# Optimization experiments

Hardware: AMD Instinct MI355X
Metric: run time of the kernel (lower is better)

## Reference

```python
import jax, jax.numpy as jnp
import numpy as np

H = 128   # hidden_size
E = 300   # embedding_dim
VOC = 32000
B, TP, TC = 8, 160, 160
D2 = 2 * H  # bidirectional feature dim


def gru_dir(x, Wih, Whh, bih, bhh, reverse):
    # x: [B,T,I] -> hidden states [B,T,Hs]; torch GRU gate order (r,z,n)
    Hs = Whh.shape[1]
    xg = jnp.einsum('bti,gi->btg', x, Wih) + bih  # [B,T,3Hs]
    if reverse:
        xg = xg[:, ::-1]
    def step(h, xt):
        gh = h @ Whh.T + bhh
        xr, xz, xn = jnp.split(xt, 3, axis=-1)
        hr, hz, hn = jnp.split(gh, 3, axis=-1)
        r = jax.nn.sigmoid(xr + hr)
        z = jax.nn.sigmoid(xz + hz)
        n = jnp.tanh(xn + r * hn)
        h = (1.0 - z) * n + z * h
        return h, h
    h0 = jnp.zeros((x.shape[0], Hs), x.dtype)
    _, hs = jax.lax.scan(step, h0, jnp.swapaxes(xg, 0, 1))
    hs = jnp.swapaxes(hs, 0, 1)
    if reverse:
        hs = hs[:, ::-1]
    return hs


def bigru(x, Wf, Uf, bif, bhf, Wb, Ub, bib, bhb):
    return jnp.concatenate([
        gru_dir(x, Wf, Uf, bif, bhf, False),
        gru_dir(x, Wb, Ub, bib, bhb, True)], axis=-1)


def setup_inputs() -> dict:
    key = jax.random.key(0)
    ks = iter(jax.random.split(key, 64))
    def rn(shape, s=0.05):
        return jax.random.normal(next(ks), shape, jnp.float32) * s
    inp = {}
    inp['text_a'] = jax.random.randint(next(ks), (B, TP), 0, VOC)
    inp['text_b'] = jax.random.randint(next(ks), (B, TC), 0, VOC)
    inp['emb'] = rn((VOC, E), 0.1)
    for pfx, ins in [('p', E), ('c', E), ('a', 6 * D2)]:
        for d in ('f', 'b'):
            inp[pfx + '_Wih_' + d] = rn((3 * H, ins))
            inp[pfx + '_Whh_' + d] = rn((3 * H, H))
            inp[pfx + '_bih_' + d] = jnp.zeros((3 * H,), jnp.float32)
            inp[pfx + '_bhh_' + d] = jnp.zeros((3 * H,), jnp.float32)
    inp['Wc1'] = rn((H, D2)); inp['Wc2'] = rn((H, D2)); inp['Vc'] = rn((H,))
    inp['Wb'] = rn((D2, D2))
    inp['Wd'] = rn((H, D2)); inp['Vd'] = rn((H,))
    inp['Wm'] = rn((H, D2)); inp['Vm'] = rn((H,))
    inp['Ws'] = rn((H, D2)); inp['Vs'] = rn((H,))
    inp['Wp'] = rn((H, D2)); inp['Vp'] = rn((H,))
    inp['W1'] = rn((H, D2)); inp['W2'] = rn((H, D2)); inp['Vv'] = rn((H,))
    inp['Wout'] = rn((2, D2)); inp['bout'] = jnp.zeros((2,), jnp.float32)
    return inp


def _forward(text_a, text_b, emb,
             p_Wih_f, p_Whh_f, p_bih_f, p_bhh_f, p_Wih_b, p_Whh_b, p_bih_b, p_bhh_b,
             c_Wih_f, c_Whh_f, c_bih_f, c_bhh_f, c_Wih_b, c_Whh_b, c_bih_b, c_bhh_b,
             a_Wih_f, a_Whh_f, a_bih_f, a_bhh_f, a_Wih_b, a_Whh_b, a_bih_b, a_bhh_b,
             Wc1, Wc2, Vc, Wb, Wd, Vd, Wm, Vm, Ws, Vs, Wp, Vp, W1, W2, Vv, Wout, bout):
    hp = bigru(emb[text_a], p_Wih_f, p_Whh_f, p_bih_f, p_bhh_f,
               p_Wih_b, p_Whh_b, p_bih_b, p_bhh_b)          # [B,Tp,2H]
    hc = bigru(emb[text_b], c_Wih_f, c_Whh_f, c_bih_f, c_bhh_f,
               c_Wih_b, c_Whh_b, c_bih_b, c_bhh_b)          # [B,Tc,2H]
    # concat (additive) attention: [B,Tc,Tp,H]
    s = jnp.tanh((hp @ Wc1.T)[:, None] + (hc @ Wc2.T)[:, :, None])
    a_cat = jax.nn.softmax(s @ Vc, axis=2)                   # [B,Tc,Tp]
    concat_rep = jnp.einsum('bct,btd->bcd', a_cat, hp)
    # bilinear attention
    a_bil = jax.nn.softmax(jnp.einsum('bcd,btd->bct', hc, hp @ Wb.T), axis=2)
    bil_rep = jnp.einsum('bct,btd->bcd', a_bil, hp)
    # dot / minus attention on [B,Tc,Tp,2H] broadcasts
    hp4 = hp[:, None]; hc4 = hc[:, :, None]
    a_dot = jax.nn.softmax(jnp.tanh((hp4 * hc4) @ Wd.T) @ Vd, axis=2)
    dot_rep = jnp.einsum('bct,btd->bcd', a_dot, hp)
    a_min = jax.nn.softmax(jnp.tanh((hp4 - hc4) @ Wm.T) @ Vm, axis=2)
    minus_rep = jnp.einsum('bct,btd->bcd', a_min, hp)
    # self attention on hc: [B,Tc,Tc,2H]
    a_self = jax.nn.softmax(jnp.tanh((hc[:, None] * hc[:, :, None]) @ Ws.T) @ Vs, axis=2)
    self_rep = jnp.einsum('bct,btd->bcd', a_self, hc)
    agg_in = jnp.concatenate([hc, self_rep, concat_rep, dot_rep, bil_rep, minus_rep], axis=-1)
    agg = bigru(agg_in, a_Wih_f, a_Whh_f, a_bih_f, a_bhh_f,
                a_Wih_b, a_Whh_b, a_bih_b, a_bhh_b)          # [B,Tc,2H]
    # pooled passage rep
    ap = jax.nn.softmax(jnp.tanh(hp @ Wp.T) @ Vp, axis=-1)   # [B,Tp]
    rp = jnp.einsum('bt,btd->bd', ap, hp)                    # [B,2H]
    # final attention over aggregation (note: no tanh, faithful to source)
    sc = (agg @ W1.T + (rp @ W2.T)[:, None]) @ Vv            # [B,Tc]
    ac = jax.nn.softmax(sc, axis=-1)
    rc = jnp.einsum('bc,bcd->bd', ac, agg)                   # [B,2H]
    return rc @ Wout.T + bout                                # [B,2] logits


def reference(text_a, text_b, emb,
              p_Wih_f, p_Whh_f, p_bih_f, p_bhh_f, p_Wih_b, p_Whh_b, p_bih_b, p_bhh_b,
              c_Wih_f, c_Whh_f, c_bih_f, c_bhh_f, c_Wih_b, c_Whh_b, c_bih_b, c_bhh_b,
              a_Wih_f, a_Whh_f, a_bih_f, a_bhh_f, a_Wih_b, a_Whh_b, a_bih_b, a_bhh_b,
              Wc1, Wc2, Vc, Wb, Wd, Vd, Wm, Vm, Ws, Vs, Wp, Vp, W1, W2, Vv, Wout, bout):
    return _forward(text_a, text_b, emb,
                    p_Wih_f, p_Whh_f, p_bih_f, p_bhh_f, p_Wih_b, p_Whh_b, p_bih_b, p_bhh_b,
                    c_Wih_f, c_Whh_f, c_bih_f, c_bhh_f, c_Wih_b, c_Whh_b, c_bih_b, c_bhh_b,
                    a_Wih_f, a_Whh_f, a_bih_f, a_bhh_f, a_Wih_b, a_Whh_b, a_bih_b, a_bhh_b,
                    Wc1, Wc2, Vc, Wb, Wd, Vd, Wm, Vm, Ws, Vs, Wp, Vp, W1, W2, Vv, Wout, bout)
```

## Files before the change

### kernel.cpp

```cpp
#include <hip/hip_runtime.h>

#define BB 8
#define TT 160
#define EE 300
#define HH 128
#define D2 256
#define G3 384
#define PSTR 40

typedef __attribute__((ext_vector_type(8))) short bf16x8;
typedef __attribute__((ext_vector_type(4))) float floatx4;

__device__ inline float fsigmoid(float x){ return 1.f/(1.f+__expf(-x)); }
__device__ inline float ftanh(float x){ return 2.f*fsigmoid(2.f*x) - 1.f; }

__device__ inline void split2(float x, unsigned short& hi, unsigned short& lo){
  unsigned ux = __float_as_uint(x);
  hi = (unsigned short)(ux>>16);
  float r = x - __uint_as_float(ux & 0xFFFF0000u);
  lo = (unsigned short)(__float_as_uint(r)>>16);
}

__global__ __launch_bounds__(256) void k_embed(const int* ta, const int* tb,
    const float* emb, float* ep, float* ec){
  const int idx = blockIdx.x*256 + threadIdx.x;
  const int per = BB*TT*EE;
  if (idx < per){
    const int e = idx % EE, bt = idx / EE;
    ep[idx] = emb[(long)ta[bt]*EE + e];
  } else {
    const int j = idx - per;
    const int e = j % EE, bt = j / EE;
    ec[j] = emb[(long)tb[bt]*EE + e];
  }
}

__global__ __launch_bounds__(256) void k_splitarr(const float* a, const float* b, int n,
    unsigned short* ahi, unsigned short* alo, unsigned short* bhi, unsigned short* blo){
  const int idx = blockIdx.x*256 + threadIdx.x;
  if (idx < n){
    split2(a[idx], ahi[idx], alo[idx]);
    split2(b[idx], bhi[idx], blo[idx]);
  }
}

struct SplitJob { const float* W; unsigned short* hi; unsigned short* lo; int n; int K; int Kp; };
struct SplitJobs { SplitJob j[12]; };

__global__ __launch_bounds__(256) void k_splitw(SplitJobs jobs){
  const SplitJob J = jobs.j[blockIdx.z];
  const int idx = blockIdx.x*256 + threadIdx.x;
  if (idx >= J.n) return;
  const int row = idx / J.Kp, k = idx - row*J.Kp;
  const float v = (k < J.K) ? J.W[(long)row*J.K + k] : 0.f;
  split2(v, J.hi[idx], J.lo[idx]);
}

struct GemmSJob {
  const float* A; const unsigned short* Whi; const unsigned short* Wlo; const float* bias;
  float* C; int N; int K; int Kp;
};
struct GemmSJobs { GemmSJob j[6]; };

__global__ __launch_bounds__(256) void k_gemmS(GemmSJobs jobs){
  const GemmSJob J = jobs.j[blockIdx.z];
  const int tid = threadIdx.x;
  const int lane = tid & 63, w = tid >> 6;
  const int l15 = lane & 15, q = lane >> 4;
  const int n0 = blockIdx.x * 64;
  if (n0 >= J.N) return;
  const int K = J.K, Kp = J.Kp;
  const long mrow = blockIdx.y*64 + w*16 + l15;
  const float* Arow = J.A + mrow*K;
  floatx4 acc[4];
  #pragma unroll
  for (int t=0;t<4;t++) acc[t] = (floatx4)0.f;
  const int nch = (K+31)>>5;
  for (int kc=0; kc<nch; kc++){
    const int k0 = kc<<5;
    const int kb = k0 + q*8;
    float av[8];
    if (k0+32 <= K){
      const floatx4 a0 = *(const floatx4*)(Arow+kb);
      const floatx4 a1 = *(const floatx4*)(Arow+kb+4);
      av[0]=a0[0];av[1]=a0[1];av[2]=a0[2];av[3]=a0[3];
      av[4]=a1[0];av[5]=a1[1];av[6]=a1[2];av[7]=a1[3];
    } else {
      #pragma unroll
      for (int j=0;j<8;j++){ const int k=kb+j; av[j] = (k<K)? Arow[k] : 0.f; }
    }
    union { bf16x8 v; unsigned short u[8]; } ahi, alo;
    #pragma unroll
    for (int j=0;j<8;j++) split2(av[j], ahi.u[j], alo.u[j]);
    #pragma unroll
    for (int t=0;t<4;t++){
      const int n = n0 + t*16 + l15;
      const long wo = (long)n*Kp + kb;
      union { bf16x8 v; uint4 d; } whi, wlo;
      whi.d = *(const uint4*)(J.Whi + wo);
      wlo.d = *(const uint4*)(J.Wlo + wo);
      acc[t] = __builtin_amdgcn_mfma_f32_16x16x32_bf16(ahi.v, whi.v, acc[t], 0,0,0);
      acc[t] = __builtin_amdgcn_mfma_f32_16x16x32_bf16(ahi.v, wlo.v, acc[t], 0,0,0);
      acc[t] = __builtin_amdgcn_mfma_f32_16x16x32_bf16(alo.v, whi.v, acc[t], 0,0,0);
    }
  }
  const long rbase = blockIdx.y*64 + w*16 + q*4;
  #pragma unroll
  for (int t=0;t<4;t++){
    const int n = n0 + t*16 + l15;
    const float bv = J.bias ? J.bias[n] : 0.f;
    #pragma unroll
    for (int r=0;r<4;r++)
      J.C[(rbase+r)*(long)J.N + n] = acc[t][r] + bv;
  }
}

struct GruJob { const float* xg; const float* Whh; const float* bhh; float* out; int ocol; int rev; };
struct GruJobs { GruJob j[4]; };

__global__ __launch_bounds__(512,1) void k_gru(GruJobs jobs){
  const GruJob J = jobs.j[blockIdx.y];
  const int bi = blockIdx.x;
  const int tid = threadIdx.x;
  const int j = tid >> 2, p = tid & 3;
  __shared__ float xgt[16][G3];
  __shared__ float hbuf[16][HH];
  __shared__ float hcur[2][HH];
  float wr[32], wz[32], wn[32];
  {
    const float* r0 = J.Whh + (long)j*HH + p*32;
    const float* z0 = J.Whh + (long)(HH+j)*HH + p*32;
    const float* n0 = J.Whh + (long)(2*HH+j)*HH + p*32;
    #pragma unroll
    for (int k=0;k<32;k+=4){
      *(floatx4*)&wr[k] = *(const floatx4*)(r0+k);
      *(floatx4*)&wz[k] = *(const floatx4*)(z0+k);
      *(floatx4*)&wn[k] = *(const floatx4*)(n0+k);
    }
  }
  float bhr=0.f,bhz=0.f,bhn=0.f;
  if (p==0){ bhr = J.bhh[j]; bhz = J.bhh[HH+j]; bhn = J.bhh[2*HH+j]; }
  if (tid < 256) ((float*)hcur)[tid] = 0.f;
  float hreg = 0.f;
  __syncthreads();

  for (int s0=0; s0<TT; s0+=16){
    #pragma unroll
    for (int r=0;r<3;r++){
      const int i = r*512 + tid;
      const int row = i/96, c4 = i - row*96;
      const int tt = J.rev ? (TT-1-(s0+row)) : (s0+row);
      *(floatx4*)&xgt[row][c4*4] = *(const floatx4*)(J.xg + ((long)bi*TT + tt)*G3 + c4*4);
    }
    __syncthreads();
    for (int si=0; si<16; si++){
      const int s = s0 + si;
      const int buf = s & 1;
      float cxr=0.f,cxz=0.f,cxn=0.f;
      if (p==0){ cxr = xgt[si][j]; cxz = xgt[si][HH+j]; cxn = xgt[si][2*HH+j]; }
      float ar=0.f, az=0.f, an=0.f;
      #pragma unroll
      for (int k=0;k<32;k+=4){
        const floatx4 h4 = *(const floatx4*)&hcur[buf][p*32+k];
        ar += wr[k]*h4[0] + wr[k+1]*h4[1] + wr[k+2]*h4[2] + wr[k+3]*h4[3];
        az += wz[k]*h4[0] + wz[k+1]*h4[1] + wz[k+2]*h4[2] + wz[k+3]*h4[3];
        an += wn[k]*h4[0] + wn[k+1]*h4[1] + wn[k+2]*h4[2] + wn[k+3]*h4[3];
      }
      ar += __shfl_xor(ar,1); ar += __shfl_xor(ar,2);
      az += __shfl_xor(az,1); az += __shfl_xor(az,2);
      an += __shfl_xor(an,1); an += __shfl_xor(an,2);
      if (p==0){
        const float gr = fsigmoid(cxr + ar + bhr);
        const float gz = fsigmoid(cxz + az + bhz);
        const float gn = ftanh  (cxn + gr*(an + bhn));
        const float h = (1.f-gz)*gn + gz*hreg;
        hreg = h;
        hcur[1-buf][j] = h;
        hbuf[si][j] = h;
      }
      __syncthreads();
    }
    {
      const int row = tid >> 5, c4 = tid & 31;
      const int tt = J.rev ? (TT-1-(s0+row)) : (s0+row);
      *(floatx4*)(J.out + ((long)bi*TT + tt)*D2 + J.ocol + c4*4) = *(const floatx4*)&hbuf[row][c4*4];
    }
  }
}

__device__ inline float block_softmax160(float s, int tid, float* red){
  float m = s;
  #pragma unroll
  for (int o=32;o>0;o>>=1) m = fmaxf(m, __shfl_xor(m,o));
  if ((tid&63)==0) red[tid>>6] = m;
  __syncthreads();
  m = fmaxf(fmaxf(red[0],red[1]), fmaxf(red[2],red[3]));
  const float p = (tid<TT) ? __expf(s-m) : 0.f;
  float t = p;
  #pragma unroll
  for (int o=32;o>0;o>>=1) t += __shfl_xor(t,o);
  if ((tid&63)==0) red[4+(tid>>6)] = t;
  __syncthreads();
  const float sum = red[4]+red[5]+red[6]+red[7];
  return p / sum;
}

__device__ inline float block_softmax160_512(float s, int tid, float* red){
  float m = s;
  #pragma unroll
  for (int o=32;o>0;o>>=1) m = fmaxf(m, __shfl_xor(m,o));
  if ((tid&63)==0) red[tid>>6] = m;
  __syncthreads();
  m = red[0];
  #pragma unroll
  for (int i=1;i<8;i++) m = fmaxf(m, red[i]);
  const float p = (tid<TT) ? __expf(s-m) : 0.f;
  float t = p;
  #pragma unroll
  for (int o=32;o>0;o>>=1) t += __shfl_xor(t,o);
  if ((tid&63)==0) red[8+(tid>>6)] = t;
  __syncthreads();
  float sum = red[8];
  #pragma unroll
  for (int i=1;i<8;i++) sum += red[8+i];
  return p / sum;
}

struct PairJob { const unsigned short* Phi; const unsigned short* Plo;
                 const float* Q; const float* W; const float* V; float* a_out; };

__global__ __launch_bounds__(512) void k_pairattn(PairJob j0, PairJob j1){
  const PairJob J = blockIdx.z ? j1 : j0;
  const int b = blockIdx.y, c = blockIdx.x;
  const int tid = threadIdx.x;
  const int lane = tid & 63, w = tid >> 6;
  const int l15 = lane & 15, q = lane >> 4;
  __shared__ unsigned short Pb[2*2*160*PSTR];
  __shared__ float Qs[D2];
  __shared__ float sc_sh[TT];
  __shared__ float red[16];
  if (tid < D2) Qs[tid] = J.Q[((long)b*TT + c)*D2 + tid];
  if (tid < TT) sc_sh[tid] = 0.f;
  const long pbase = (long)b*TT*D2;

  int s_hl[5], s_t[5], s_d4[5];
  #pragma unroll
  for (int r=0;r<5;r++){
    const int idx = tid + r*512;
    const int hl = (idx >= 1280) ? 1 : 0;
    const int e4 = idx - hl*1280;
    s_hl[r] = hl; s_t[r] = e4 >> 3; s_d4[r] = e4 & 7;
  }
  uint2 stg[5];
  #pragma unroll
  for (int r=0;r<5;r++){
    const unsigned short* src = (s_hl[r] ? J.Plo : J.Phi) + pbase + (long)s_t[r]*D2 + s_d4[r]*4;
    stg[r] = *(const uint2*)src;
  }
  const float* Wbase = J.W + (long)(w*16 + l15)*D2;
  floatx4 wv0 = *(const floatx4*)(Wbase + q*8);
  floatx4 wv1 = *(const floatx4*)(Wbase + q*8 + 4);
  #pragma unroll
  for (int r=0;r<5;r++)
    *(uint2*)&Pb[((0*2 + s_hl[r])*160 + s_t[r])*PSTR + s_d4[r]*4] = stg[r];
  __syncthreads();

  floatx4 acc[10];
  #pragma unroll
  for (int nt=0;nt<10;nt++) acc[nt] = (floatx4)0.f;

  for (int kc=0; kc<8; kc++){
    const floatx4 wc0 = wv0, wc1 = wv1;
    if (kc < 7){
      wv0 = *(const floatx4*)(Wbase + (kc+1)*32 + q*8);
      wv1 = *(const floatx4*)(Wbase + (kc+1)*32 + q*8 + 4);
      #pragma unroll
      for (int r=0;r<5;r++){
        const unsigned short* src = (s_hl[r] ? J.Plo : J.Phi) + pbase + (long)s_t[r]*D2 + (kc+1)*32 + s_d4[r]*4;
        stg[r] = *(const uint2*)src;
      }
    }
    const int d0 = kc*32 + q*8;
    const floatx4 q0 = *(const floatx4*)&Qs[d0];
    const floatx4 q1 = *(const floatx4*)&Qs[d0+4];
    union { bf16x8 v; unsigned short u[8]; } ah, al;
    #pragma unroll
    for (int j=0;j<4;j++){
      split2(wc0[j]*q0[j], ah.u[j],   al.u[j]);
      split2(wc1[j]*q1[j], ah.u[4+j], al.u[4+j]);
    }
    const int buf = kc & 1;
    #pragma unroll
    for (int nt=0;nt<10;nt++){
      const int t = nt*16 + l15;
      union { bf16x8 v; } bh, bl;
      bh.v = *(const bf16x8*)&Pb[((buf*2+0)*160 + t)*PSTR + q*8];
      bl.v = *(const bf16x8*)&Pb[((buf*2+1)*160 + t)*PSTR + q*8];
      acc[nt] = __builtin_amdgcn_mfma_f32_16x16x32_bf16(ah.v, bh.v, acc[nt], 0,0,0);
      acc[nt] = __builtin_amdgcn_mfma_f32_16x16x32_bf16(ah.v, bl.v, acc[nt], 0,0,0);
      acc[nt] = __builtin_amdgcn_mfma_f32_16x16x32_bf16(al.v, bh.v, acc[nt], 0,0,0);
    }
    if (kc < 7){
      const int nbuf = 1 - buf;
      #pragma unroll
      for (int r=0;r<5;r++)
        *(uint2*)&Pb[((nbuf*2 + s_hl[r])*160 + s_t[r])*PSTR + s_d4[r]*4] = stg[r];
      __syncthreads();
    }
  }

  float vreg[4];
  #pragma unroll
  for (int r=0;r<4;r++) vreg[r] = J.V[w*16 + q*4 + r];
  #pragma unroll
  for (int nt=0;nt<10;nt++){
    float pp = 0.f;
    #pragma unroll
    for (int r=0;r<4;r++) pp += vreg[r]*ftanh(acc[nt][r]);
    pp += __shfl_xor(pp,16);
    pp += __shfl_xor(pp,32);
    if (q==0) atomicAdd(&sc_sh[nt*16 + l15], pp);
  }
  __syncthreads();
  const float s = (tid<TT)? sc_sh[tid] : -INFINITY;
  const float a = block_softmax160_512(s, tid, red);
  if (tid < TT) J.a_out[((long)b*TT + c)*TT + tid] = a;
}

struct AddJob { const float* up; const float* uc; const float* V; float sgn; float* a_out; };

__global__ __launch_bounds__(256) void k_addattn(AddJob j0, AddJob j1){
  const AddJob J = blockIdx.z ? j1 : j0;
  const int b = blockIdx.y, c = blockIdx.x, tid = threadIdx.x;
  __shared__ float ucc[HH];
  __shared__ float vv[HH];
  __shared__ float red[8];
  if (tid < HH){
    ucc[tid] = J.sgn * J.uc[((long)b*TT + c)*HH + tid];
    vv[tid] = J.V[tid];
  }
  __syncthreads();
  float s = -INFINITY;
  if (tid < TT){
    const float* ur = J.up + ((long)b*TT + tid)*HH;
    float a0 = 0.f;
    #pragma unroll 4
    for (int k=0;k<HH;k++) a0 += vv[k]*ftanh(ur[k]+ucc[k]);
    s = a0;
  }
  const float a = block_softmax160(s, tid, red);
  if (tid < TT) J.a_out[((long)b*TT + c)*TT + tid] = a;
}

__global__ __launch_bounds__(256) void k_bilattn(const float* hc, const float* hpWb, float* a_out){
  const int b = blockIdx.y, c = blockIdx.x, tid = threadIdx.x;
  __shared__ float hcc[D2];
  __shared__ float red[8];
  if (tid < D2) hcc[tid] = hc[((long)b*TT + c)*D2 + tid];
  __syncthreads();
  float s = -INFINITY;
  if (tid < TT){
    const float* pr = hpWb + ((long)b*TT + tid)*D2;
    float a0 = 0.f;
    #pragma unroll 4
    for (int k=0;k<D2;k++) a0 += hcc[k]*pr[k];
    s = a0;
  }
  const float a = block_softmax160(s, tid, red);
  if (tid < TT) a_out[((long)b*TT + c)*TT + tid] = a;
}

__global__ __launch_bounds__(256) void k_rep(const float* hp, const float* hc,
    const float* acat, const float* abil, const float* adot, const float* amin, const float* aself,
    float* aggin){
  const int b = blockIdx.y, c = blockIdx.x, tid = threadIdx.x;
  __shared__ float a5[5][TT];
  {
    const long base = ((long)b*TT + c)*TT;
    for (int i=tid;i<5*TT;i+=256){
      const int which = i/TT, t = i - which*TT;
      const float* p = which==0? acat : which==1? abil : which==2? adot : which==3? amin : aself;
      a5[which][t] = p[base + t];
    }
  }
  __syncthreads();
  const float* hpb = hp + (long)b*TT*D2 + tid;
  const float* hcb = hc + (long)b*TT*D2 + tid;
  float r0=0.f,r1=0.f,r2=0.f,r3=0.f,r4=0.f;
  for (int t=0;t<TT;t++){
    const float vp = hpb[(long)t*D2];
    const float vc = hcb[(long)t*D2];
    r0 += a5[0][t]*vp;
    r1 += a5[1][t]*vp;
    r2 += a5[2][t]*vp;
    r3 += a5[3][t]*vp;
    r4 += a5[4][t]*vc;
  }
  float* o = aggin + ((long)b*TT + c)*(6*D2);
  o[tid]        = hc[((long)b*TT + c)*D2 + tid];
  o[D2 + tid]   = r4;
  o[2*D2 + tid] = r0;
  o[3*D2 + tid] = r2;
  o[4*D2 + tid] = r1;
  o[5*D2 + tid] = r3;
}

__global__ __launch_bounds__(256) void k_tail1(const float* upP, const float* Vp,
    const float* hp, float* rp){
  const int b = blockIdx.x, tid = threadIdx.x;
  __shared__ float vv[HH];
  __shared__ float ap_sh[TT];
  __shared__ float red[8];
  if (tid<HH) vv[tid] = Vp[tid];
  __syncthreads();
  float s = -INFINITY;
  if (tid<TT){
    const float* ur = upP + ((long)b*TT + tid)*HH;
    float a0=0.f;
    #pragma unroll 4
    for (int k=0;k<HH;k++) a0 += vv[k]*ftanh(ur[k]);
    s = a0;
  }
  const float a = block_softmax160(s, tid, red);
  if (tid<TT) ap_sh[tid] = a;
  __syncthreads();
  float acc = 0.f;
  const float* hpb = hp + (long)b*TT*D2 + tid;
  for (int t=0;t<TT;t++) acc += ap_sh[t]*hpb[(long)t*D2];
  rp[b*D2 + tid] = acc;
}

__global__ __launch_bounds__(256) void k_tail2(const float* aggW1, const float* agg, const float* rp,
    const float* W2, const float* Vv, const float* Wout, const float* bout,
    float* out){
  const int b = blockIdx.x, tid = threadIdx.x;
  __shared__ float rpw[HH];
  __shared__ float ac_sh[TT];
  __shared__ float rc_sh[D2];
  __shared__ float red[8];
  if (tid < HH){
    float a0=0.f;
    const float* wr2 = W2 + (long)tid*D2;
    const float* rr = rp + b*D2;
    for (int d=0; d<D2; d++) a0 += wr2[d]*rr[d];
    rpw[tid] = a0;
  }
  __syncthreads();
  float s = -INFINITY;
  if (tid < TT){
    const float* ar = aggW1 + ((long)b*TT + tid)*HH;
    float a0=0.f;
    for (int k=0;k<HH;k++) a0 += Vv[k]*(ar[k] + rpw[k]);
    s = a0;
  }
  const float a = block_softmax160(s, tid, red);
  if (tid < TT) ac_sh[tid] = a;
  __syncthreads();
  float rc=0.f;
  const float* ab = agg + (long)b*TT*D2 + tid;
  for (int t=0;t<TT;t++) rc += ac_sh[t]*ab[(long)t*D2];
  rc_sh[tid] = rc;
  __syncthreads();
  if (tid < 2){
    float o = bout[tid];
    const float* wr = Wout + (long)tid*D2;
    for (int d=0; d<D2; d++) o += wr[d]*rc_sh[d];
    out[b*2 + tid] = o;
  }
}

extern "C" void kernel_launch(void* const* d_in, const int* in_sizes, int n_in,
                              void* d_out, int out_size, void* d_ws, size_t ws_size,
                              hipStream_t stream){
  (void)in_sizes; (void)n_in; (void)out_size; (void)ws_size;
  const int* ta = (const int*)d_in[0];
  const int* tb = (const int*)d_in[1];
  const float* emb = (const float*)d_in[2];
  #define F32(i) ((const float*)d_in[i])

  float* ws = (float*)d_ws;
  float* ep    = ws;
  float* ec    = ep    + 384000;
  float* xg_pf = ec    + 384000;
  float* xg_pb = xg_pf + 491520;
  float* xg_cf = xg_pb + 491520;
  float* xg_cb = xg_cf + 491520;
  float* hp    = xg_cb + 491520;
  float* hc    = hp    + 327680;
  float* up1   = hc    + 327680;
  float* uc2   = up1   + 163840;
  float* ump   = uc2   + 163840;
  float* umc   = ump   + 163840;
  float* upP   = umc   + 163840;
  float* hpWb  = upP   + 163840;
  float* acat  = hpWb  + 327680;
  float* abil  = acat  + 204800;
  float* adot  = abil  + 204800;
  float* amin  = adot  + 204800;
  float* aself = amin  + 204800;
  float* aggin = aself + 204800;
  float* rp    = aggin + 1966080;
  unsigned short* hp_hi = (unsigned short*)(rp + 2048);
  unsigned short* hp_lo = hp_hi + 327680;
  unsigned short* hc_hi = hp_lo + 327680;
  unsigned short* hc_lo = hc_hi + 327680;
  unsigned short* wsp = hc_lo + 327680;
  unsigned short* w3h  = wsp;             unsigned short* w3l  = w3h  + 122880;
  unsigned short* w7h  = w3l  + 122880;   unsigned short* w7l  = w7h  + 122880;
  unsigned short* w11h = w7l  + 122880;   unsigned short* w11l = w11h + 122880;
  unsigned short* w15h = w11l + 122880;   unsigned short* w15l = w15h + 122880;
  unsigned short* w27h = w15l + 122880;   unsigned short* w27l = w27h + 32768;
  unsigned short* w28h = w27l + 32768;    unsigned short* w28l = w28h + 32768;
  unsigned short* w33h = w28l + 32768;    unsigned short* w33l = w33h + 32768;
  unsigned short* w37h = w33l + 32768;    unsigned short* w37l = w37h + 32768;
  unsigned short* w30h = w37l + 32768;    unsigned short* w30l = w30h + 65536;
  unsigned short* w19h = w30l + 65536;    unsigned short* w19l = w19h + 589824;
  unsigned short* w23h = w19l + 589824;   unsigned short* w23l = w23h + 589824;
  unsigned short* w39h = w23l + 589824;   unsigned short* w39l = w39h + 32768;
  float* xg_af = xg_pf;
  float* xg_ab = xg_pb;
  float* agg   = xg_cf;
  float* aggW1 = xg_cb;

  k_embed<<<dim3(3000), dim3(256), 0, stream>>>(ta, tb, emb, ep, ec);
  SplitJobs sj = {};
  sj.j[0]  = {F32(3),  w3h,  w3l,  122880, 300, 320};
  sj.j[1]  = {F32(7),  w7h,  w7l,  122880, 300, 320};
  sj.j[2]  = {F32(11), w11h, w11l, 122880, 300, 320};
  sj.j[3]  = {F32(15), w15h, w15l, 122880, 300, 320};
  sj.j[4]  = {F32(27), w27h, w27l, 32768,  256, 256};
  sj.j[5]  = {F32(28), w28h, w28l, 32768,  256, 256};
  sj.j[6]  = {F32(33), w33h, w33l, 32768,  256, 256};
  sj.j[7]  = {F32(37), w37h, w37l, 32768,  256, 256};
  sj.j[8]  = {F32(30), w30h, w30l, 65536,  256, 256};
  sj.j[9]  = {F32(19), w19h, w19l, 589824, 1536, 1536};
  sj.j[10] = {F32(23), w23h, w23l, 589824, 1536, 1536};
  sj.j[11] = {F32(39), w39h, w39l, 32768,  256, 256};
  k_splitw<<<dim3(2304,1,12), dim3(256), 0, stream>>>(sj);

  GemmSJobs ja = {};
  ja.j[0] = {ep, w3h,  w3l,  F32(5),  xg_pf, 384, 300, 320};
  ja.j[1] = {ep, w7h,  w7l,  F32(9),  xg_pb, 384, 300, 320};
  ja.j[2] = {ec, w11h, w11l, F32(13), xg_cf, 384, 300, 320};
  ja.j[3] = {ec, w15h, w15l, F32(17), xg_cb, 384, 300, 320};
  k_gemmS<<<dim3(6,20,4), dim3(256), 0, stream>>>(ja);

  GruJobs gj = {};
  gj.j[0] = {xg_pf, F32(4),  F32(6),  hp, 0,   0};
  gj.j[1] = {xg_pb, F32(8),  F32(10), hp, 128, 1};
  gj.j[2] = {xg_cf, F32(12), F32(14), hc, 0,   0};
  gj.j[3] = {xg_cb, F32(16), F32(18), hc, 128, 1};
  k_gru<<<dim3(8,4), dim3(512), 0, stream>>>(gj);

  k_splitarr<<<dim3(1280), dim3(256), 0, stream>>>(hp, hc, 327680, hp_hi, hp_lo, hc_hi, hc_lo);

  GemmSJobs jb = {};
  jb.j[0] = {hp, w27h, w27l, nullptr, up1,  128, 256, 256};
  jb.j[1] = {hc, w28h, w28l, nullptr, uc2,  128, 256, 256};
  jb.j[2] = {hp, w33h, w33l, nullptr, ump,  128, 256, 256};
  jb.j[3] = {hc, w33h, w33l, nullptr, umc,  128, 256, 256};
  jb.j[4] = {hp, w37h, w37l, nullptr, upP,  128, 256, 256};
  jb.j[5] = {hp, w30h, w30l, nullptr, hpWb, 256, 256, 256};
  k_gemmS<<<dim3(4,20,6), dim3(256), 0, stream>>>(jb);

  PairJob pd  = {hp_hi, hp_lo, hc, F32(31), F32(32), adot};
  PairJob psf = {hc_hi, hc_lo, hc, F32(35), F32(36), aself};
  k_pairattn<<<dim3(160,8,2), dim3(512), 0, stream>>>(pd, psf);

  AddJob ac_ = {up1, uc2, F32(29),  1.f, acat};
  AddJob am_ = {ump, umc, F32(34), -1.f, amin};
  k_addattn<<<dim3(160,8,2), dim3(256), 0, stream>>>(ac_, am_);

  k_bilattn<<<dim3(160,8), dim3(256), 0, stream>>>(hc, hpWb, abil);

  k_tail1<<<dim3(8), dim3(256), 0, stream>>>(upP, F32(38), hp, rp);

  k_rep<<<dim3(160,8), dim3(256), 0, stream>>>(hp, hc, acat, abil, adot, amin, aself, aggin);

  GemmSJobs jc = {};
  jc.j[0] = {aggin, w19h, w19l, F32(21), xg_af, 384, 1536, 1536};
  jc.j[1] = {aggin, w23h, w23l, F32(25), xg_ab, 384, 1536, 1536};
  k_gemmS<<<dim3(6,20,2), dim3(256), 0, stream>>>(jc);

  GruJobs gja = {};
  gja.j[0] = {xg_af, F32(20), F32(22), agg, 0,   0};
  gja.j[1] = {xg_ab, F32(24), F32(26), agg, 128, 1};
  k_gru<<<dim3(8,2), dim3(512), 0, stream>>>(gja);

  GemmSJobs jd = {};
  jd.j[0] = {agg, w39h, w39l, nullptr, aggW1, 128, 256, 256};
  k_gemmS<<<dim3(2,20,1), dim3(256), 0, stream>>>(jd);

  k_tail2<<<dim3(8), dim3(256), 0, stream>>>(aggW1, agg, rp, F32(40), F32(41), F32(42), F32(43),
                                             (float*)d_out);
  #undef F32
}
```

Measured before the change: 835.9 us.

## Batch GRU recurrence across all sequences with split-bf16 MFMA per direction

The GRU kernel now runs one block per direction that processes all 8 batch rows together. The hidden-state matvec is replaced by 16x16x32 bf16 MFMAs using hi/lo split of weights and hidden state for near-fp32 accuracy. The xg staging chunk shrinks to 2 timesteps. This aims to cut the per-step scalar FMA and shuffle-reduction cost, but it uses far fewer blocks (4 and 2 instead of 32 and 16), puts half the lanes idle in the gate epilogue, and adds a barrier per 2-step chunk load.

```diff
diff --git a/kernel.cpp b/kernel.cpp
--- a/kernel.cpp
+++ b/kernel.cpp
@@ -115,75 +115,108 @@
   }
 }
 
+#define GCH 2
 struct GruJob { const float* xg; const float* Whh; const float* bhh; float* out; int ocol; int rev; };
 struct GruJobs { GruJob j[4]; };
 
 __global__ __launch_bounds__(512,1) void k_gru(GruJobs jobs){
-  const GruJob J = jobs.j[blockIdx.y];
-  const int bi = blockIdx.x;
+  const GruJob J = jobs.j[blockIdx.x];
   const int tid = threadIdx.x;
-  const int j = tid >> 2, p = tid & 3;
-  __shared__ float xgt[16][G3];
-  __shared__ float hbuf[16][HH];
-  __shared__ float hcur[2][HH];
-  float wr[32], wz[32], wn[32];
-  {
-    const float* r0 = J.Whh + (long)j*HH + p*32;
-    const float* z0 = J.Whh + (long)(HH+j)*HH + p*32;
-    const float* n0 = J.Whh + (long)(2*HH+j)*HH + p*32;
-    #pragma unroll
-    for (int k=0;k<32;k+=4){
-      *(floatx4*)&wr[k] = *(const floatx4*)(r0+k);
-      *(floatx4*)&wz[k] = *(const floatx4*)(z0+k);
-      *(floatx4*)&wn[k] = *(const floatx4*)(n0+k);
-    }
-  }
-  float bhr=0.f,bhz=0.f,bhn=0.f;
-  if (p==0){ bhr = J.bhh[j]; bhz = J.bhh[HH+j]; bhn = J.bhh[2*HH+j]; }
-  if (tid < 256) ((float*)hcur)[tid] = 0.f;
-  float hreg = 0.f;
-  __syncthreads();
-
-  for (int s0=0; s0<TT; s0+=16){
-    #pragma unroll
-    for (int r=0;r<3;r++){
-      const int i = r*512 + tid;
-      const int row = i/96, c4 = i - row*96;
-      const int tt = J.rev ? (TT-1-(s0+row)) : (s0+row);
-      *(floatx4*)&xgt[row][c4*4] = *(const floatx4*)(J.xg + ((long)bi*TT + tt)*G3 + c4*4);
+  const int lane = tid & 63, w = tid >> 6;
+  const int l15 = lane & 15, q = lane >> 4;
+  const int b = l15 & 7;
+  const bool act = (l15 < 8);
+  __shared__ float xgt[GCH][BB][G3];
+  __shared__ float hbuf[GCH][BB][HH];
+  __shared__ unsigned short hhi[2][BB][HH];
+  __shared__ unsigned short hlo[2][BB][HH];
+
+  union BF { bf16x8 v; unsigned short u[8]; uint4 d; };
+  BF Ah[3][4], Al[3][4];
+  #pragma unroll
+  for (int g=0; g<3; g++){
+    const float* wr = J.Whh + (long)(g*HH + w*16 + l15)*HH;
+    #pragma unroll
+    for (int kc=0; kc<4; kc++){
+      const floatx4 w0 = *(const floatx4*)(wr + kc*32 + q*8);
+      const floatx4 w1 = *(const floatx4*)(wr + kc*32 + q*8 + 4);
+      #pragma unroll
+      for (int jj=0; jj<4; jj++){
+        split2(w0[jj], Ah[g][kc].u[jj],   Al[g][kc].u[jj]);
+        split2(w1[jj], Ah[g][kc].u[4+jj], Al[g][kc].u[4+jj]);
+      }
+    }
+  }
+  const int u0 = w*16 + q*4;
+  const floatx4 bhr = *(const floatx4*)(J.bhh + u0);
+  const floatx4 bhz = *(const floatx4*)(J.bhh + HH + u0);
+  const floatx4 bhn = *(const floatx4*)(J.bhh + 2*HH + u0);
+  floatx4 hreg = (floatx4)0.f;
+  for (int i = tid; i < BB*HH; i += 512){
+    ((unsigned*)hhi)[i] = 0u;
+    ((unsigned*)hlo)[i] = 0u;
+  }
+  __syncthreads();
+
+  for (int c0=0; c0<TT; c0+=GCH){
+    #pragma unroll
+    for (int it=0; it<3; it++){
+      const int idx = it*512 + tid;
+      const int si = idx/768, rem = idx - si*768;
+      const int bb = rem/96, c4 = rem - bb*96;
+      const int tt = J.rev ? (TT-1-(c0+si)) : (c0+si);
+      *(floatx4*)&xgt[si][bb][c4*4] = *(const floatx4*)(J.xg + ((long)bb*TT + tt)*G3 + c4*4);
     }
     __syncthreads();
-    for (int si=0; si<16; si++){
-      const int s = s0 + si;
+    #pragma unroll
+    for (int si=0; si<GCH; si++){
+      const int s = c0 + si;
       const int buf = s & 1;
-      float cxr=0.f,cxz=0.f,cxn=0.f;
-      if (p==0){ cxr = xgt[si][j]; cxz = xgt[si][HH+j]; cxn = xgt[si][2*HH+j]; }
-      float ar=0.f, az=0.f, an=0.f;
+      floatx4 accr=(floatx4)0.f, accz=(floatx4)0.f, accn=(floatx4)0.f;
       #pragma unroll
-      for (int k=0;k<32;k+=4){
-        const floatx4 h4 = *(const floatx4*)&hcur[buf][p*32+k];
-        ar += wr[k]*h4[0] + wr[k+1]*h4[1] + wr[k+2]*h4[2] + wr[k+3]*h4[3];
-        az += wz[k]*h4[0] + wz[k+1]*h4[1] + wz[k+2]*h4[2] + wz[k+3]*h4[3];
-        an += wn[k]*h4[0] + wn[k+1]*h4[1] + wn[k+2]*h4[2] + wn[k+3]*h4[3];
+      for (int kc=0; kc<4; kc++){
+        BF Bh, Bl;
+        Bh.d = *(const uint4*)&hhi[buf][b][kc*32 + q*8];
+        Bl.d = *(const uint4*)&hlo[buf][b][kc*32 + q*8];
+        accr = __builtin_amdgcn_mfma_f32_16x16x32_bf16(Ah[0][kc].v, Bh.v, accr, 0,0,0);
+        accz = __builtin_amdgcn_mfma_f32_16x16x32_bf16(Ah[1][kc].v, Bh.v, accz, 0,0,0);
+        accn = __builtin_amdgcn_mfma_f32_16x16x32_bf16(Ah[2][kc].v, Bh.v, accn, 0,0,0);
+        accr = __builtin_amdgcn_mfma_f32_16x16x32_bf16(Ah[0][kc].v, Bl.v, accr, 0,0,0);
+        accz = __builtin_amdgcn_mfma_f32_16x16x32_bf16(Ah[1][kc].v, Bl.v, accz, 0,0,0);
+        accn = __builtin_amdgcn_mfma_f32_16x16x32_bf16(Ah[2][kc].v, Bl.v, accn, 0,0,0);
+        accr = __builtin_amdgcn_mfma_f32_16x16x32_bf16(Al[0][kc].v, Bh.v, accr, 0,0,0);
+        accz = __builtin_amdgcn_mfma_f32_16x16x32_bf16(Al[1][kc].v, Bh.v, accz, 0,0,0);
+        accn = __builtin_amdgcn_mfma_f32_16x16x32_bf16(Al[2][kc].v, Bh.v, accn, 0,0,0);
       }
-      ar += __shfl_xor(ar,1); ar += __shfl_xor(ar,2);
-      az += __shfl_xor(az,1); az += __shfl_xor(az,2);
-      an += __shfl_xor(an,1); an += __shfl_xor(an,2);
-      if (p==0){
-        const float gr = fsigmoid(cxr + ar + bhr);
-        const float gz = fsigmoid(cxz + az + bhz);
-        const float gn = ftanh  (cxn + gr*(an + bhn));
-        const float h = (1.f-gz)*gn + gz*hreg;
-        hreg = h;
-        hcur[1-buf][j] = h;
-        hbuf[si][j] = h;
+      if (act){
+        const float* xb = &xgt[si][b][0];
+        const floatx4 cxr = *(const floatx4*)(xb + u0);
+        const floatx4 cxz = *(const floatx4*)(xb + HH + u0);
+        const floatx4 cxn = *(const floatx4*)(xb + 2*HH + u0);
+        floatx4 hnew;
+        union { unsigned short u[4]; uint2 d; } h4, l4;
+        #pragma unroll
+        for (int r=0; r<4; r++){
+          const float gr = fsigmoid(cxr[r] + accr[r] + bhr[r]);
+          const float gz = fsigmoid(cxz[r] + accz[r] + bhz[r]);
+          const float gn = ftanh  (cxn[r] + gr*(accn[r] + bhn[r]));
+          hnew[r] = (1.f-gz)*gn + gz*hreg[r];
+          split2(hnew[r], h4.u[r], l4.u[r]);
+        }
+        hreg = hnew;
+        const int nbuf = 1 - buf;
+        *(uint2*)&hhi[nbuf][b][u0] = h4.d;
+        *(uint2*)&hlo[nbuf][b][u0] = l4.d;
+        *(floatx4*)&hbuf[si][b][u0] = hnew;
       }
       __syncthreads();
     }
     {
-      const int row = tid >> 5, c4 = tid & 31;
-      const int tt = J.rev ? (TT-1-(s0+row)) : (s0+row);
-      *(floatx4*)(J.out + ((long)bi*TT + tt)*D2 + J.ocol + c4*4) = *(const floatx4*)&hbuf[row][c4*4];
+      const int idx = tid;
+      const int si = idx >> 8, rem = idx & 255;
+      const int bb = rem >> 5, c4 = rem & 31;
+      const int tt = J.rev ? (TT-1-(c0+si)) : (c0+si);
+      *(floatx4*)(J.out + ((long)bb*TT + tt)*D2 + J.ocol + c4*4) = *(const floatx4*)&hbuf[si][bb][c4*4];
     }
   }
 }
@@ -550,7 +583,7 @@
   gj.j[1] = {xg_pb, F32(8),  F32(10), hp, 128, 1};
   gj.j[2] = {xg_cf, F32(12), F32(14), hc, 0,   0};
   gj.j[3] = {xg_cb, F32(16), F32(18), hc, 128, 1};
-  k_gru<<<dim3(8,4), dim3(512), 0, stream>>>(gj);
+  k_gru<<<dim3(4), dim3(512), 0, stream>>>(gj);
 
   k_splitarr<<<dim3(1280), dim3(256), 0, stream>>>(hp, hc, 327680, hp_hi, hp_lo, hc_hi, hc_lo);
 
@@ -585,7 +618,7 @@
   GruJobs gja = {};
   gja.j[0] = {xg_af, F32(20), F32(22), agg, 0,   0};
   gja.j[1] = {xg_ab, F32(24), F32(26), agg, 128, 1};
-  k_gru<<<dim3(8,2), dim3(512), 0, stream>>>(gja);
+  k_gru<<<dim3(2), dim3(512), 0, stream>>>(gja);
 
   GemmSJobs jd = {};
   jd.j[0] = {agg, w39h, w39l, nullptr, aggW1, 128, 256, 256};
```

New measurement: 1.283 ms. 53.5% more time.

## Tile additive attention over 16 queries per block with shared-memory staging

Applied to the files above, without the earlier changes.

The additive attention kernel now handles 16 query rows per block instead of one. It stages 16x128 tiles of the key projections in LDS and computes a 16x16 score tile per pass, so each key row is reused across 16 queries instead of being reloaded from global memory by every block. Softmax is done with 16-lane shuffle reductions, and uncoalesced per-thread row reads are replaced by vectorized LDS reads. The tail kernel also caches rp in shared memory and vectorizes the W2 loads. The grid drops from 2560 to 160 blocks, which reduces parallelism on a large GPU, and the tanh work per block rises to 16 queries.

```diff
diff --git a/kernel.cpp b/kernel.cpp
--- a/kernel.cpp
+++ b/kernel.cpp
@@ -331,25 +331,50 @@
 
 __global__ __launch_bounds__(256) void k_addattn(AddJob j0, AddJob j1){
   const AddJob J = blockIdx.z ? j1 : j0;
-  const int b = blockIdx.y, c = blockIdx.x, tid = threadIdx.x;
-  __shared__ float ucc[HH];
+  const int b = blockIdx.y, c0 = blockIdx.x*16, tid = threadIdx.x;
+  const int ci = tid >> 4, tj = tid & 15;
+  __shared__ float ucc[16][132];
+  __shared__ float up_sh[16][132];
   __shared__ float vv[HH];
-  __shared__ float red[8];
-  if (tid < HH){
-    ucc[tid] = J.sgn * J.uc[((long)b*TT + c)*HH + tid];
-    vv[tid] = J.V[tid];
-  }
-  __syncthreads();
-  float s = -INFINITY;
-  if (tid < TT){
-    const float* ur = J.up + ((long)b*TT + tid)*HH;
+  __shared__ float sc[16][TT];
+  if (tid < HH) vv[tid] = J.V[tid];
+  for (int i = tid; i < 16*HH; i += 256){
+    const int cc = i >> 7, k = i & 127;
+    ucc[cc][k] = J.sgn * J.uc[((long)b*TT + c0 + cc)*HH + k];
+  }
+  __syncthreads();
+  for (int tch = 0; tch < 10; tch++){
+    for (int i = tid; i < 16*HH; i += 256){
+      const int tt = i >> 7, k = i & 127;
+      up_sh[tt][k] = J.up[((long)b*TT + tch*16 + tt)*HH + k];
+    }
+    __syncthreads();
     float a0 = 0.f;
     #pragma unroll 4
-    for (int k=0;k<HH;k++) a0 += vv[k]*ftanh(ur[k]+ucc[k]);
-    s = a0;
-  }
-  const float a = block_softmax160(s, tid, red);
-  if (tid < TT) J.a_out[((long)b*TT + c)*TT + tid] = a;
+    for (int k = 0; k < HH; k += 4){
+      const floatx4 u4 = *(const floatx4*)&up_sh[tj][k];
+      const floatx4 c4 = *(const floatx4*)&ucc[ci][k];
+      a0 += vv[k]*ftanh(u4[0]+c4[0]) + vv[k+1]*ftanh(u4[1]+c4[1])
+          + vv[k+2]*ftanh(u4[2]+c4[2]) + vv[k+3]*ftanh(u4[3]+c4[3]);
+    }
+    sc[ci][tch*16 + tj] = a0;
+    __syncthreads();
+  }
+  float m = -INFINITY;
+  float sv[10];
+  #pragma unroll
+  for (int u = 0; u < 10; u++){ sv[u] = sc[ci][tj + 16*u]; m = fmaxf(m, sv[u]); }
+  #pragma unroll
+  for (int o = 8; o >= 1; o >>= 1) m = fmaxf(m, __shfl_xor(m, o));
+  float ssum = 0.f;
+  #pragma unroll
+  for (int u = 0; u < 10; u++){ sv[u] = __expf(sv[u] - m); ssum += sv[u]; }
+  #pragma unroll
+  for (int o = 8; o >= 1; o >>= 1) ssum += __shfl_xor(ssum, o);
+  const float inv = 1.f / ssum;
+  float* ao = J.a_out + ((long)b*TT + c0 + ci)*TT + tj;
+  #pragma unroll
+  for (int u = 0; u < 10; u++) ao[16*u] = sv[u]*inv;
 }
 
 __global__ __launch_bounds__(256) void k_bilattn(const float* hc, const float* hpWb, float* a_out){
@@ -434,15 +459,20 @@
     const float* W2, const float* Vv, const float* Wout, const float* bout,
     float* out){
   const int b = blockIdx.x, tid = threadIdx.x;
+  __shared__ float rps[D2];
   __shared__ float rpw[HH];
   __shared__ float ac_sh[TT];
   __shared__ float rc_sh[D2];
   __shared__ float red[8];
+  if (tid < D2) rps[tid] = rp[b*D2 + tid];
+  __syncthreads();
   if (tid < HH){
     float a0=0.f;
     const float* wr2 = W2 + (long)tid*D2;
-    const float* rr = rp + b*D2;
-    for (int d=0; d<D2; d++) a0 += wr2[d]*rr[d];
+    for (int d=0; d<D2; d+=4){
+      const floatx4 w4 = *(const floatx4*)(wr2 + d);
+      a0 += w4[0]*rps[d] + w4[1]*rps[d+1] + w4[2]*rps[d+2] + w4[3]*rps[d+3];
+    }
     rpw[tid] = a0;
   }
   __syncthreads();
@@ -569,7 +599,7 @@
 
   AddJob ac_ = {up1, uc2, F32(29),  1.f, acat};
   AddJob am_ = {ump, umc, F32(34), -1.f, amin};
-  k_addattn<<<dim3(160,8,2), dim3(256), 0, stream>>>(ac_, am_);
+  k_addattn<<<dim3(10,8,2), dim3(256), 0, stream>>>(ac_, am_);
 
   k_bilattn<<<dim3(160,8), dim3(256), 0, stream>>>(hc, hpWb, abil);
 
```

After: 838.2 us. No clear change (+0.3%).
